# Optimization experiments

Hardware: AMD Instinct MI355X
Metric: run time of the kernel (lower is better)

## Reference

```python
import jax, jax.numpy as jnp
import numpy as np

B, S, D, H, F = 2, 2048, 768, 12, 3072
DH = D // H  # head dim = 64


def setup_inputs() -> dict:
    key = jax.random.key(0)
    ks = jax.random.split(key, 16)
    sc = 0.02
    p = {
        "src": jax.random.normal(ks[0], (B, S, D), jnp.float32),
        # attention projections (torch Linear layout: [out, in], bias=True in xformers MultiHeadDispatch)
        "wq": jax.random.normal(ks[1], (D, D), jnp.float32) * sc,
        "bq": jnp.zeros((D,), jnp.float32),
        "wk": jax.random.normal(ks[2], (D, D), jnp.float32) * sc,
        "bk": jnp.zeros((D,), jnp.float32),
        "wv": jax.random.normal(ks[3], (D, D), jnp.float32) * sc,
        "bv": jnp.zeros((D,), jnp.float32),
        "wo": jax.random.normal(ks[4], (D, D), jnp.float32) * sc,
        "bo": jnp.zeros((D,), jnp.float32),
        # FFN: fc1 (bias) -> SwiGLU (two bias-free F->F projections) -> fc2 (bias)
        "w_fc1": jax.random.normal(ks[5], (F, D), jnp.float32) * sc,
        "b_fc1": jnp.zeros((F,), jnp.float32),
        "w_in": jax.random.normal(ks[6], (F, F), jnp.float32) * sc,
        "w_gate": jax.random.normal(ks[7], (F, F), jnp.float32) * sc,
        "w_fc2": jax.random.normal(ks[8], (D, F), jnp.float32) * sc,
        "b_fc2": jnp.zeros((D,), jnp.float32),
        # RMSNorm weights
        "g_attn": jnp.ones((D,), jnp.float32),
        "g_ffn": jnp.ones((D,), jnp.float32),
    }
    return p


def _rmsnorm(x, g):
    eps = jnp.asarray(jnp.finfo(x.dtype).eps, x.dtype)
    return x * jax.lax.rsqrt(jnp.mean(x * x, axis=-1, keepdims=True) + eps) * g


def _rope_cos_sin(seq_len, dim, dtype):
    # xformers RotaryEmbedding: inv_freq over even indices, emb = cat(freqs, freqs)
    inv_freq = 1.0 / (10000.0 ** (jnp.arange(0, dim, 2, dtype=jnp.float32) / dim))
    freqs = jnp.arange(seq_len, dtype=jnp.float32)[:, None] * inv_freq[None, :]  # [S, dim/2]
    emb = jnp.concatenate([freqs, freqs], axis=-1)  # [S, dim]
    return jnp.cos(emb).astype(dtype), jnp.sin(emb).astype(dtype)


def _rotate_half(x):
    x1, x2 = jnp.split(x, 2, axis=-1)
    return jnp.concatenate([-x2, x1], axis=-1)


def _apply_rope(x, cos, sin):
    # x: [B, H, S, DH]; cos/sin: [S, DH]
    return x * cos[None, None] + _rotate_half(x) * sin[None, None]


def _block(src, wq, bq, wk, bk, wv, bv, wo, bo,
           w_fc1, b_fc1, w_in, w_gate, w_fc2, b_fc2, g_attn, g_ffn):
    b, s, d = src.shape
    x = _rmsnorm(src, g_attn)
    q = (x @ wq.T + bq).reshape(b, s, H, DH).transpose(0, 2, 1, 3)
    k = (x @ wk.T + bk).reshape(b, s, H, DH).transpose(0, 2, 1, 3)
    v = (x @ wv.T + bv).reshape(b, s, H, DH).transpose(0, 2, 1, 3)
    cos, sin = _rope_cos_sin(s, DH, x.dtype)
    q = _apply_rope(q, cos, sin)
    k = _apply_rope(k, cos, sin)
    scale = 1.0 / np.sqrt(DH)
    scores = jnp.einsum("bhsd,bhtd->bhst", q * scale, k)  # non-causal, no mask
    attn = jax.nn.softmax(scores, axis=-1)
    ctx = jnp.einsum("bhst,bhtd->bhsd", attn, v)
    ctx = ctx.transpose(0, 2, 1, 3).reshape(b, s, d)
    attn_out = ctx @ wo.T + bo

    y = _rmsnorm(src + attn_out, g_ffn)
    h = y @ w_fc1.T + b_fc1
    h = (h @ w_in.T) * jax.nn.silu(h @ w_gate.T)  # SwiGLU
    ffn_out = h @ w_fc2.T + b_fc2
    return y + ffn_out


def reference(src, wq, bq, wk, bk, wv, bv, wo, bo,
              w_fc1, b_fc1, w_in, w_gate, w_fc2, b_fc2, g_attn, g_ffn):
    return _block(src, wq, bq, wk, bk, wv, bv, wo, bo,
                  w_fc1, b_fc1, w_in, w_gate, w_fc2, b_fc2, g_attn, g_ffn)
```

## Files before the change

kernel.cpp:

```cpp
#include <hip/hip_runtime.h>

#define DEV static __device__ __forceinline__

typedef __attribute__((ext_vector_type(8))) short bf16x8;
typedef __attribute__((ext_vector_type(4))) short short4v;
typedef __attribute__((ext_vector_type(4))) float f32x4;

DEV f32x4 mfma16(bf16x8 a, bf16x8 b, f32x4 c){
  return __builtin_amdgcn_mfma_f32_16x16x32_bf16(a, b, c, 0, 0, 0);
}
DEV float bf2f(short s){ union{unsigned u; float f;} v; v.u=((unsigned)(unsigned short)s)<<16; return v.f; }
DEV short f2bf(float f){ union{float f; unsigned u;} v; v.f=f; unsigned r=v.u+0x7fffu+((v.u>>16)&1u); return (short)(r>>16); }
DEV void gload16(const void* g, void* l){
  __builtin_amdgcn_global_load_lds((const __attribute__((address_space(1))) void*)g,
                                   (__attribute__((address_space(3))) void*)l, 16, 0, 0);
}
DEV int cvtpk(float lo, float hi){
  int r; asm("v_cvt_pk_bf16_f32 %0, %1, %2" : "=v"(r) : "v"(lo), "v"(hi)); return r;
}

enum { EPI_QKV=4 };

__global__ void k_csmall(const float* __restrict__ p0, const float* __restrict__ p1,
                         const float* __restrict__ p2, const float* __restrict__ p3,
                         short* __restrict__ dst){
  int v = blockIdx.x * 256 + threadIdx.x;
  const float* src; int rel;
  if      (v < 147456){ src=p0; rel=v; }
  else if (v < 294912){ src=p1; rel=v-147456; }
  else if (v < 442368){ src=p2; rel=v-294912; }
  else                { src=p3; rel=v-442368; }
  float4 x = ((const float4*)src)[rel];
  short4v o; o.x=f2bf(x.x); o.y=f2bf(x.y); o.z=f2bf(x.z); o.w=f2bf(x.w);
  ((short4v*)dst)[v] = o;
}

__global__ void k_rmsnorm(const float* __restrict__ x, const float* __restrict__ g,
                          short* __restrict__ out){
  int row = blockIdx.x*4 + (threadIdx.x>>6);
  int lane = threadIdx.x & 63;
  const float* xr = x + (size_t)row*768;
  float4 v[3];
  float ss = 0.f;
  #pragma unroll
  for (int i=0;i<3;i++){
    v[i] = *(const float4*)(xr + i*256 + lane*4);
    ss += v[i].x*v[i].x + v[i].y*v[i].y + v[i].z*v[i].z + v[i].w*v[i].w;
  }
  #pragma unroll
  for (int d=32; d>0; d>>=1) ss += __shfl_xor(ss, d);
  float sc = rsqrtf(ss*(1.f/768.f) + 1.1920929e-7f);
  #pragma unroll
  for (int i=0;i<3;i++){
    int c0 = i*256 + lane*4;
    float4 gv = *(const float4*)(g + c0);
    short4v o;
    o.x = f2bf(v[i].x*sc*gv.x); o.y = f2bf(v[i].y*sc*gv.y);
    o.z = f2bf(v[i].z*sc*gv.z); o.w = f2bf(v[i].w*sc*gv.w);
    *(short4v*)(out + (size_t)row*768 + c0) = o;
  }
}

template<int EPI>
__launch_bounds__(256, 2)
__global__ void k_gemm(const short* __restrict__ Aptr, const short* __restrict__ Bptr,
                       void* __restrict__ Cout, const float* __restrict__ bias,
                       const void* __restrict__ aux, const float* __restrict__ bias2,
                       const float* __restrict__ bias3, const void* __restrict__ aux2,
                       int M, int N, int K){
  __shared__ short ldsA[128*32];
  __shared__ short ldsB[128*32];
  const int t = threadIdx.x;
  const int wave = t >> 6, lane = t & 63;
  const int l15 = lane & 15, l4 = lane >> 4;
  const int nwg = gridDim.x * gridDim.y;
  const int bid0 = blockIdx.y * gridDim.x + blockIdx.x;
  const int cpx = nwg >> 3;
  const int bid = (bid0 & 7) * cpx + (bid0 >> 3);
  const int bm = bid / gridDim.x, bn = bid % gridDim.x;
  const int wr = wave >> 1, wc = wave & 1;

  f32x4 acc[4][4] = {};

  const short* Ag = Aptr + (size_t)(bm*128 + wave*32 + (lane>>2))*K + (lane&3)*8;
  const short* Bg = Bptr + (size_t)(bn*128 + wave*32 + (lane>>2))*K + (lane&3)*8;
  short* lA = ldsA + wave*1024;
  short* lB = ldsB + wave*1024;

  for (int k0 = 0; k0 < K; k0 += 32){
    __syncthreads();
    gload16(Ag + k0,                lA);
    gload16(Ag + k0 + 16*(size_t)K, lA + 512);
    gload16(Bg + k0,                lB);
    gload16(Bg + k0 + 16*(size_t)K, lB + 512);
    __syncthreads();
    bf16x8 af[4], bfr[4];
    #pragma unroll
    for (int m=0;m<4;m++) af[m]  = *(const bf16x8*)(ldsA + (wr*64 + m*16 + l15)*32 + l4*8);
    #pragma unroll
    for (int n=0;n<4;n++) bfr[n] = *(const bf16x8*)(ldsB + (wc*64 + n*16 + l15)*32 + l4*8);
    #pragma unroll
    for (int m=0;m<4;m++)
      #pragma unroll
      for (int n=0;n<4;n++)
        acc[m][n] = mfma16(af[m], bfr[n], acc[m][n]);
  }

  const int row0 = bm*128 + wr*64;
  const int col0 = bn*128 + wc*64;

  if constexpr (EPI == EPI_QKV){
    const int proj = col0 / 768;
    const int c768 = col0 - proj*768;
    const int h = c768 >> 6;
    const float* bs = proj==0 ? bias : (proj==1 ? bias2 : bias3);
    float bvv[4];
    #pragma unroll
    for (int n=0;n<4;n++) bvv[n] = bs[c768 + n*16 + l15];
    if (proj == 2){
      short* Ov = (short*)const_cast<void*>(aux2);
      #pragma unroll
      for (int m=0;m<4;m++){
        #pragma unroll
        for (int j=0;j<4;j++){
          int row = row0 + m*16 + l4*4 + j;
          int b = row >> 11, s = row & 2047;
          size_t hb = (size_t)(b*12 + h)*64;
          #pragma unroll
          for (int n=0;n<4;n++)
            Ov[(hb + n*16 + l15)*2048 + s] = f2bf(acc[m][n][j] + bvv[n]);
        }
      }
    } else {
      short* O = proj==0 ? (short*)Cout : (short*)const_cast<void*>(aux);
      const float sc = proj==0 ? 0.18033688011112042f : 1.0f;
      const float RC = 0.41524101186092034f;
      float invf0 = exp2f(-(float)l15 * RC);
      float invf1 = exp2f(-(float)(16 + l15) * RC);
      #pragma unroll
      for (int m=0;m<4;m++){
        #pragma unroll
        for (int j=0;j<4;j++){
          int row = row0 + m*16 + l4*4 + j;
          int b = row >> 11, s = row & 2047;
          size_t obase = ((size_t)(b*12 + h)*2048 + (size_t)s)*64;
          float a0 = acc[m][0][j] + bvv[0];
          float a1 = acc[m][1][j] + bvv[1];
          float a2 = acc[m][2][j] + bvv[2];
          float a3 = acc[m][3][j] + bvv[3];
          float sn0, cs0, sn1, cs1;
          __sincosf((float)s * invf0, &sn0, &cs0);
          __sincosf((float)s * invf1, &sn1, &cs1);
          O[obase + l15]      = f2bf((a0*cs0 - a2*sn0)*sc);
          O[obase + 16 + l15] = f2bf((a1*cs1 - a3*sn1)*sc);
          O[obase + 32 + l15] = f2bf((a2*cs0 + a0*sn0)*sc);
          O[obase + 48 + l15] = f2bf((a3*cs1 + a1*sn1)*sc);
        }
      }
    }
  }
}

__launch_bounds__(256, 4)
__global__ void k_fatA(const short* __restrict__ Q, const short* __restrict__ Kb,
                       const short* __restrict__ Vb, short* __restrict__ ctx,
                       const float* __restrict__ winf, const float* __restrict__ wgf,
                       const float* __restrict__ wfc2f, short* __restrict__ dstbig,
                       const float* __restrict__ wfc1, short* __restrict__ wfc1T){
  __shared__ short shm[16384];
  const int id = blockIdx.x;
  const int tid = threadIdx.x;

  if (id < 768){
    const int wave = tid>>6, lane = tid&63;
    const int l15 = lane&15, l4 = lane>>4;
    const int qt = id & 31, bh = id >> 5;
    const short* Qh  = Q  + (size_t)bh*2048*64;
    const short* Kh  = Kb + (size_t)bh*2048*64;
    const short* Vth = Vb + (size_t)bh*64*2048;

    const int r7  = lane>>3;
    const int swz = ((lane&7) ^ r7) << 3;
    const int rr0 = wave*8 + r7, rr1 = 32 + wave*8 + r7;
    const size_t kOff0 = (size_t)rr0*64   + swz, kOff1 = (size_t)rr1*64   + swz;
    const size_t vOff0 = (size_t)rr0*2048 + swz, vOff1 = (size_t)rr1*2048 + swz;

    bf16x8 qf[2];
    #pragma unroll
    for (int kf=0;kf<2;kf++)
      qf[kf] = *(const bf16x8*)(Qh + (size_t)(qt*64 + wave*16 + l15)*64 + kf*32 + l4*8);

    f32x4 cacc[4] = {};
    f32x4 lacc = {};
    union { int w[4]; bf16x8 v; } onesf;
    onesf.w[0] = onesf.w[1] = onesf.w[2] = onesf.w[3] = 0x3F803F80;

    #define STAGE(sel, kv0) do { \
      const short* ksp = Kh + (size_t)(kv0)*64; \
      const short* vsp = Vth + (kv0); \
      short* kd = shm + (sel)*4096 + wave*512; \
      short* vd = shm + 8192 + (sel)*4096 + wave*512; \
      gload16(ksp + kOff0, kd); \
      gload16(ksp + kOff1, kd + 2048); \
      gload16(vsp + vOff0, vd); \
      gload16(vsp + vOff1, vd + 2048); \
    } while(0)

    STAGE(0, 0);

    for (int tt = 0; tt < 32; ++tt){
      const int cur = tt & 1;
      if (tt < 31){
        STAGE(cur^1, (tt+1)*64);
        asm volatile("s_waitcnt vmcnt(4)" ::: "memory");
      } else {
        asm volatile("s_waitcnt vmcnt(0)" ::: "memory");
      }
      __builtin_amdgcn_sched_barrier(0);
      __builtin_amdgcn_s_barrier();
      __builtin_amdgcn_sched_barrier(0);

      const short* KtC = shm + cur*4096;
      const short* VtC = shm + 8192 + cur*4096;

      f32x4 sacc[4] = {};
      __builtin_amdgcn_s_setprio(1);
      #pragma unroll
      for (int kf=0;kf<2;kf++){
        #pragma unroll
        for (int mk=0;mk<4;mk++){
          int r = mk*16 + l15;
          bf16x8 kfr = *(const bf16x8*)(KtC + r*64 + (((kf*4+l4) ^ (l15&7))<<3));
          sacc[mk] = mfma16(kfr, qf[kf], sacc[mk]);
        }
      }
      __builtin_amdgcn_s_setprio(0);

      int pk01[4], pk23[4];
      #pragma unroll
      for (int mk=0;mk<4;mk++){
        float p0 = exp2f(sacc[mk][0]);
        float p1 = exp2f(sacc[mk][1]);
        float p2 = exp2f(sacc[mk][2]);
        float p3 = exp2f(sacc[mk][3]);
        pk01[mk] = cvtpk(p0, p1);
        pk23[mk] = cvtpk(p2, p3);
      }

      #pragma unroll
      for (int ks=0;ks<2;ks++){
        int srcA = l15 + ((l4&1)<<5);
        int srcB = srcA + 16;
        int hi = l4>>1;
        int w0a = __shfl(pk01[2*ks], srcA), w0b = __shfl(pk01[2*ks+1], srcA);
        int w1a = __shfl(pk23[2*ks], srcA), w1b = __shfl(pk23[2*ks+1], srcA);
        int w2a = __shfl(pk01[2*ks], srcB), w2b = __shfl(pk01[2*ks+1], srcB);
        int w3a = __shfl(pk23[2*ks], srcB), w3b = __shfl(pk23[2*ks+1], srcB);
        union { int w[4]; bf16x8 v; } pa;
        pa.w[0] = hi ? w0b : w0a;
        pa.w[1] = hi ? w1b : w1a;
        pa.w[2] = hi ? w2b : w2a;
        pa.w[3] = hi ? w3b : w3a;
        __builtin_amdgcn_s_setprio(1);
        #pragma unroll
        for (int nf=0;nf<4;nf++){
          int dh = nf*16 + l15;
          bf16x8 vf = *(const bf16x8*)(VtC + dh*64 + (((ks*4+l4) ^ (dh&7))<<3));
          cacc[nf] = mfma16(pa.v, vf, cacc[nf]);
        }
        lacc = mfma16(pa.v, onesf.v, lacc);
        __builtin_amdgcn_s_setprio(0);
      }

      __builtin_amdgcn_sched_barrier(0);
      __builtin_amdgcn_s_barrier();
    }
    #undef STAGE

    const int b = bh/12, h = bh%12;
    #pragma unroll
    for (int j=0;j<4;j++){
      float inv = 1.f / lacc[j];
      int s = qt*64 + wave*16 + l4*4 + j;
      size_t base = ((size_t)b*2048 + s)*768 + h*64;
      #pragma unroll
      for (int nf=0;nf<4;nf++)
        ctx[base + nf*16 + l15] = f2bf(cacc[nf][j] * inv);
    }
  } else if (id < 21504){
    int v = (id - 768)*256 + tid;
    const float* src; int rel;
    if      (v < 2359296){ src=winf;  rel=v; }
    else if (v < 4718592){ src=wgf;   rel=v-2359296; }
    else                 { src=wfc2f; rel=v-4718592; }
    float4 x = ((const float4*)src)[rel];
    short4v o; o.x=f2bf(x.x); o.y=f2bf(x.y); o.z=f2bf(x.z); o.w=f2bf(x.w);
    ((short4v*)dstbig)[v] = o;
  } else {
    int idx = id - 21504;
    int f0 = (idx % 96)*32, d0 = (idx / 96)*32;
    float* lt = (float*)shm;
    int r = tid >> 3, c4 = tid & 7;
    float4 v = *(const float4*)(wfc1 + (size_t)(f0 + r)*768 + d0 + c4*4);
    lt[r*33 + c4*4+0] = v.x; lt[r*33 + c4*4+1] = v.y;
    lt[r*33 + c4*4+2] = v.z; lt[r*33 + c4*4+3] = v.w;
    __syncthreads();
    short4v o;
    o.x = f2bf(lt[(c4*4+0)*33 + r]);
    o.y = f2bf(lt[(c4*4+1)*33 + r]);
    o.z = f2bf(lt[(c4*4+2)*33 + r]);
    o.w = f2bf(lt[(c4*4+3)*33 + r]);
    *(short4v*)(wfc1T + (size_t)(d0 + r)*3072 + f0 + c4*4) = o;
  }
}

__launch_bounds__(256, 2)
__global__ void k_fatB(const short* __restrict__ ctxb, const short* __restrict__ wo_b,
                       float* __restrict__ resid, const float* __restrict__ bo,
                       const float* __restrict__ srcf,
                       const short* __restrict__ win_b, const short* __restrict__ wfc1T,
                       short* __restrict__ Pw,
                       const float* __restrict__ bfc1, float* __restrict__ bvg){
  __shared__ short shm[8192];
  const int id = blockIdx.x;
  const int t = threadIdx.x;
  const int wave = t >> 6, lane = t & 63;
  const int l15 = lane & 15, l4 = lane >> 4;
  const int wr = wave >> 1, wc = wave & 1;
  short* lA = shm + wave*1024;
  short* lB = shm + 4096 + wave*1024;

  if (id < 192){
    const int bid = (id & 7)*24 + (id >> 3);
    const int bm = bid / 6, bn = bid % 6;
    f32x4 acc[4][4] = {};
    const short* Ag = ctxb + (size_t)(bm*128 + wave*32 + (lane>>2))*768 + (lane&3)*8;
    const short* Bg = wo_b + (size_t)(bn*128 + wave*32 + (lane>>2))*768 + (lane&3)*8;
    for (int k0 = 0; k0 < 768; k0 += 32){
      __syncthreads();
      gload16(Ag + k0,          lA);
      gload16(Ag + k0 + 16*768, lA + 512);
      gload16(Bg + k0,          lB);
      gload16(Bg + k0 + 16*768, lB + 512);
      __syncthreads();
      bf16x8 af[4], bfr[4];
      #pragma unroll
      for (int m=0;m<4;m++) af[m]  = *(const bf16x8*)(shm + (wr*64 + m*16 + l15)*32 + l4*8);
      #pragma unroll
      for (int n=0;n<4;n++) bfr[n] = *(const bf16x8*)(shm + 4096 + (wc*64 + n*16 + l15)*32 + l4*8);
      #pragma unroll
      for (int m=0;m<4;m++)
        #pragma unroll
        for (int n=0;n<4;n++)
          acc[m][n] = mfma16(af[m], bfr[n], acc[m][n]);
    }
    const int row0 = bm*128 + wr*64;
    const int col0 = bn*128 + wc*64;
    float bvv[4];
    #pragma unroll
    for (int n=0;n<4;n++) bvv[n] = bo[col0 + n*16 + l15];
    #pragma unroll
    for (int m=0;m<4;m++)
      #pragma unroll
      for (int j=0;j<4;j++){
        size_t rb = (size_t)(row0 + m*16 + l4*4 + j)*768 + col0 + l15;
        #pragma unroll
        for (int n=0;n<4;n++) resid[rb + n*16] = acc[m][n][j] + bvv[n] + srcf[rb + n*16];
      }
  } else if (id < 768){
    const int id2 = id - 192;
    const int z = id2 / 288;
    const int rest = id2 - z*288;
    const int koff = z * 1536;
    const int bid = (rest & 7)*36 + (rest >> 3);
    const int bm = bid / 6, bn = bid % 6;
    f32x4 acc[4][4] = {};
    const short* Ag = win_b + (size_t)(bm*128 + wave*32 + (lane>>2))*3072 + (lane&3)*8 + koff;
    const short* Bg = wfc1T + (size_t)(bn*128 + wave*32 + (lane>>2))*3072 + (lane&3)*8 + koff;
    for (int k0 = 0; k0 < 1536; k0 += 32){
      __syncthreads();
      gload16(Ag + k0,           lA);
      gload16(Ag + k0 + 16*3072, lA + 512);
      gload16(Bg + k0,           lB);
      gload16(Bg + k0 + 16*3072, lB + 512);
      __syncthreads();
      bf16x8 af[4], bfr[4];
      #pragma unroll
      for (int m=0;m<4;m++) af[m]  = *(const bf16x8*)(shm + (wr*64 + m*16 + l15)*32 + l4*8);
      #pragma unroll
      for (int n=0;n<4;n++) bfr[n] = *(const bf16x8*)(shm + 4096 + (wc*64 + n*16 + l15)*32 + l4*8);
      #pragma unroll
      for (int m=0;m<4;m++)
        #pragma unroll
        for (int n=0;n<4;n++)
          acc[m][n] = mfma16(af[m], bfr[n], acc[m][n]);
    }
    short* Pz = Pw + (size_t)z * 4718592;
    const int row0 = bm*128 + wr*64;
    const int col0 = bn*128 + wc*64;
    #pragma unroll
    for (int m=0;m<4;m++)
      #pragma unroll
      for (int j=0;j<4;j++){
        size_t rb = (size_t)(row0 + m*16 + l4*4 + j)*768 + col0 + l15;
        #pragma unroll
        for (int n=0;n<4;n++) Pz[rb + n*16] = f2bf(acc[m][n][j]);
      }
  } else {
    int row = (id - 768)*4 + wave;
    const short* wrow = win_b + (size_t)row*3072 + lane*48;
    const float* bb = bfc1 + lane*48;
    float s = 0.f;
    #pragma unroll
    for (int i=0;i<6;i++){
      bf16x8 w = *(const bf16x8*)(wrow + i*8);
      float4 b0 = *(const float4*)(bb + i*8);
      float4 b1 = *(const float4*)(bb + i*8 + 4);
      s += bf2f(w[0])*b0.x + bf2f(w[1])*b0.y + bf2f(w[2])*b0.z + bf2f(w[3])*b0.w
         + bf2f(w[4])*b1.x + bf2f(w[5])*b1.y + bf2f(w[6])*b1.z + bf2f(w[7])*b1.w;
    }
    #pragma unroll
    for (int d=32; d>0; d>>=1) s += __shfl_xor(s, d);
    if (lane == 0) bvg[row] = s;
  }
}

__global__ void k_fatC(const float* __restrict__ resid, const float* __restrict__ gffn,
                       short* __restrict__ yb,
                       const short* __restrict__ Pw, short* __restrict__ comp){
  const int id = blockIdx.x;
  if (id < 1024){
    int row = id*4 + (threadIdx.x>>6);
    int lane = threadIdx.x & 63;
    const float* xr = resid + (size_t)row*768;
    float4 v[3];
    float ss = 0.f;
    #pragma unroll
    for (int i=0;i<3;i++){
      v[i] = *(const float4*)(xr + i*256 + lane*4);
      ss += v[i].x*v[i].x + v[i].y*v[i].y + v[i].z*v[i].z + v[i].w*v[i].w;
    }
    #pragma unroll
    for (int d=32; d>0; d>>=1) ss += __shfl_xor(ss, d);
    float sc = rsqrtf(ss*(1.f/768.f) + 1.1920929e-7f);
    #pragma unroll
    for (int i=0;i<3;i++){
      int c0 = i*256 + lane*4;
      float4 gv = *(const float4*)(gffn + c0);
      short4v o;
      o.x = f2bf(v[i].x*sc*gv.x); o.y = f2bf(v[i].y*sc*gv.y);
      o.z = f2bf(v[i].z*sc*gv.z); o.w = f2bf(v[i].w*sc*gv.w);
      *(short4v*)(yb + (size_t)row*768 + c0) = o;
    }
  } else {
    int i = (id - 1024)*256 + threadIdx.x;
    short4v a = ((const short4v*)Pw)[i];
    short4v b = ((const short4v*)(Pw + 4718592))[i];
    short4v o;
    o.x = f2bf(bf2f(a.x) + bf2f(b.x)); o.y = f2bf(bf2f(a.y) + bf2f(b.y));
    o.z = f2bf(bf2f(a.z) + bf2f(b.z)); o.w = f2bf(bf2f(a.w) + bf2f(b.w));
    ((short4v*)comp)[i] = o;
  }
}

__launch_bounds__(256, 2)
__global__ void k_part(const short* __restrict__ Aptr, const short* __restrict__ Bptr,
                       short* __restrict__ Pa, short* __restrict__ Pb){
  __shared__ short ldsA[128*32];
  __shared__ short ldsB[128*32];
  const int t = threadIdx.x;
  const int wave = t >> 6, lane = t & 63;
  const int l15 = lane & 15, l4 = lane >> 4;
  const int K = 3072;
  const int z = blockIdx.z;
  const int koff = z * 768;
  const int bid0 = blockIdx.y * 6 + blockIdx.x;
  const int bid = (bid0 & 7) * 24 + (bid0 >> 3);
  const int bm = bid / 6, bn = bid % 6;
  const int wr = wave >> 1, wc = wave & 1;

  f32x4 acc[4][4] = {};

  const short* Ag = Aptr + (size_t)(bm*128 + wave*32 + (lane>>2))*K + (lane&3)*8 + koff;
  const short* Bg = Bptr + (size_t)(bn*128 + wave*32 + (lane>>2))*K + (lane&3)*8 + koff;
  short* lA = ldsA + wave*1024;
  short* lB = ldsB + wave*1024;

  for (int k0 = 0; k0 < 768; k0 += 32){
    __syncthreads();
    gload16(Ag + k0,                lA);
    gload16(Ag + k0 + 16*(size_t)K, lA + 512);
    gload16(Bg + k0,                lB);
    gload16(Bg + k0 + 16*(size_t)K, lB + 512);
    __syncthreads();
    bf16x8 af[4], bfr[4];
    #pragma unroll
    for (int m=0;m<4;m++) af[m]  = *(const bf16x8*)(ldsA + (wr*64 + m*16 + l15)*32 + l4*8);
    #pragma unroll
    for (int n=0;n<4;n++) bfr[n] = *(const bf16x8*)(ldsB + (wc*64 + n*16 + l15)*32 + l4*8);
    #pragma unroll
    for (int m=0;m<4;m++)
      #pragma unroll
      for (int n=0;n<4;n++)
        acc[m][n] = mfma16(af[m], bfr[n], acc[m][n]);
  }

  short* P = (z < 2) ? (Pa + (size_t)z*3145728) : (Pb + (size_t)(z-2)*3145728);
  const int row0 = bm*128 + wr*64;
  const int col0 = bn*128 + wc*64;
  #pragma unroll
  for (int m=0;m<4;m++)
    #pragma unroll
    for (int j=0;j<4;j++){
      size_t rb = (size_t)(row0 + m*16 + l4*4 + j)*768 + col0 + l15;
      #pragma unroll
      for (int n=0;n<4;n++) P[rb + n*16] = f2bf(acc[m][n][j]);
    }
}

__global__ void k_fc2red(const short* __restrict__ Pa, const short* __restrict__ Pb,
                         const float* __restrict__ bias, const short* __restrict__ yv,
                         float* __restrict__ out){
  int i = blockIdx.x * 256 + threadIdx.x;
  short4v a = ((const short4v*)Pa)[i];
  short4v b = ((const short4v*)(Pa + 3145728))[i];
  short4v c = ((const short4v*)Pb)[i];
  short4v d = ((const short4v*)(Pb + 3145728))[i];
  float4 bv = *(const float4*)(bias + (i % 192)*4);
  short4v y = ((const short4v*)yv)[i];
  float4 o;
  o.x = bf2f(a.x) + bf2f(b.x) + bf2f(c.x) + bf2f(d.x) + bv.x + bf2f(y.x);
  o.y = bf2f(a.y) + bf2f(b.y) + bf2f(c.y) + bf2f(d.y) + bv.y + bf2f(y.y);
  o.z = bf2f(a.z) + bf2f(b.z) + bf2f(c.z) + bf2f(d.z) + bv.z + bf2f(y.z);
  o.w = bf2f(a.w) + bf2f(b.w) + bf2f(c.w) + bf2f(d.w) + bv.w + bf2f(y.w);
  ((float4*)out)[i] = o;
}

__launch_bounds__(256, 2)
__global__ void k_ffglu(const short* __restrict__ Aptr, const short* __restrict__ Wcomp,
                        const float* __restrict__ bvg, short* __restrict__ Cout){
  __shared__ short lds[3*12288];
  const int tid = threadIdx.x;
  const int wave = tid >> 6, lane = tid & 63;
  const int l15 = lane & 15, l4 = lane >> 4;
  const int wm = wave >> 1, wn = wave & 1;
  const int K = 768, N = 3072;
  const int nt = 24;

  const int lin = blockIdx.y * 48 + blockIdx.x;
  const int xcd = lin & 7, idx = lin >> 3;
  const int bm = ((xcd & 1) << 3) + idx / 12;
  const int bn = (xcd >> 1) * 12 + idx % 12;

  const int srcC = ((lane & 3) ^ ((lane >> 3) & 3)) * 8;

  const short* aSrc[4];
  int aDst[4];
  #pragma unroll
  for (int i=0;i<4;i++){
    int s = i*4 + wave;
    int row = s*16 + (lane>>2);
    aSrc[i] = Aptr + (size_t)(bm*256 + row)*K + srcC;
    aDst[i] = s*512;
  }
  const short* bSrc[2];
  int bDst[2];
  #pragma unroll
  for (int i=0;i<2;i++){
    int j = i*4 + wave;
    int pidx = (j>>1)*16 + (lane>>2);
    int grow = (j & 1) ? 3072 : 0;
    bSrc[i] = Wcomp + (size_t)(grow + bn*64 + pidx)*K + srcC;
    bDst[i] = 8192 + j*512;
  }

  int offA[8], offB[4];
  #pragma unroll
  for (int m=0;m<8;m++){
    int r = wm*128 + m*16 + l15;
    offA[m] = r*32 + ((l4 ^ ((l15>>1)&3))<<3);
  }
  #pragma unroll
  for (int nf=0;nf<4;nf++){
    int r = wn*64 + nf*16 + l15;
    offB[nf] = 8192 + r*32 + ((l4 ^ ((l15>>1)&3))<<3);
  }

  f32x4 accv[8][2] = {};
  f32x4 accg[8][2] = {};

  short *b0 = lds, *b1 = lds + 12288, *b2 = lds + 24576;

  #define GSTAGE_ALL(buf, t) do{ \
    gload16(aSrc[0] + (size_t)(t)*32, (buf) + aDst[0]); \
    gload16(aSrc[1] + (size_t)(t)*32, (buf) + aDst[1]); \
    gload16(aSrc[2] + (size_t)(t)*32, (buf) + aDst[2]); \
    gload16(aSrc[3] + (size_t)(t)*32, (buf) + aDst[3]); \
    gload16(bSrc[0] + (size_t)(t)*32, (buf) + bDst[0]); \
    gload16(bSrc[1] + (size_t)(t)*32, (buf) + bDst[1]); \
  }while(0)

  GSTAGE_ALL(b0, 0);
  GSTAGE_ALL(b1, 1);

  for (int t = 0; t < nt; ++t){
    if (t < nt-1){
      asm volatile("s_waitcnt vmcnt(6)" ::: "memory");
    } else {
      asm volatile("s_waitcnt vmcnt(0)" ::: "memory");
    }
    __builtin_amdgcn_sched_barrier(0);
    __builtin_amdgcn_s_barrier();
    __builtin_amdgcn_sched_barrier(0);

    if (t + 2 < nt) GSTAGE_ALL(b2, t+2);

    bf16x8 a0 = *(const bf16x8*)(b0 + offA[0]);
    bf16x8 a1 = *(const bf16x8*)(b0 + offA[1]);
    bf16x8 a2 = *(const bf16x8*)(b0 + offA[2]);
    bf16x8 a3 = *(const bf16x8*)(b0 + offA[3]);
    bf16x8 a4 = *(const bf16x8*)(b0 + offA[4]);
    bf16x8 a5 = *(const bf16x8*)(b0 + offA[5]);
    bf16x8 a6 = *(const bf16x8*)(b0 + offA[6]);
    bf16x8 a7 = *(const bf16x8*)(b0 + offA[7]);
    bf16x8 v0 = *(const bf16x8*)(b0 + offB[0]);
    bf16x8 g0 = *(const bf16x8*)(b0 + offB[1]);
    bf16x8 v1 = *(const bf16x8*)(b0 + offB[2]);
    bf16x8 g1 = *(const bf16x8*)(b0 + offB[3]);

    __builtin_amdgcn_s_setprio(1);
    accv[0][0] = mfma16(a0, v0, accv[0][0]);  accg[0][0] = mfma16(a0, g0, accg[0][0]);
    accv[1][0] = mfma16(a1, v0, accv[1][0]);  accg[1][0] = mfma16(a1, g0, accg[1][0]);
    accv[2][0] = mfma16(a2, v0, accv[2][0]);  accg[2][0] = mfma16(a2, g0, accg[2][0]);
    accv[3][0] = mfma16(a3, v0, accv[3][0]);  accg[3][0] = mfma16(a3, g0, accg[3][0]);
    accv[0][1] = mfma16(a0, v1, accv[0][1]);  accg[0][1] = mfma16(a0, g1, accg[0][1]);
    accv[1][1] = mfma16(a1, v1, accv[1][1]);  accg[1][1] = mfma16(a1, g1, accg[1][1]);
    accv[2][1] = mfma16(a2, v1, accv[2][1]);  accg[2][1] = mfma16(a2, g1, accg[2][1]);
    accv[3][1] = mfma16(a3, v1, accv[3][1]);  accg[3][1] = mfma16(a3, g1, accg[3][1]);
    accv[4][0] = mfma16(a4, v0, accv[4][0]);  accg[4][0] = mfma16(a4, g0, accg[4][0]);
    accv[5][0] = mfma16(a5, v0, accv[5][0]);  accg[5][0] = mfma16(a5, g0, accg[5][0]);
    accv[6][0] = mfma16(a6, v0, accv[6][0]);  accg[6][0] = mfma16(a6, g0, accg[6][0]);
    accv[7][0] = mfma16(a7, v0, accv[7][0]);  accg[7][0] = mfma16(a7, g0, accg[7][0]);
    accv[4][1] = mfma16(a4, v1, accv[4][1]);  accg[4][1] = mfma16(a4, g1, accg[4][1]);
    accv[5][1] = mfma16(a5, v1, accv[5][1]);  accg[5][1] = mfma16(a5, g1, accg[5][1]);
    accv[6][1] = mfma16(a6, v1, accv[6][1]);  accg[6][1] = mfma16(a6, g1, accg[6][1]);
    accv[7][1] = mfma16(a7, v1, accv[7][1]);  accg[7][1] = mfma16(a7, g1, accg[7][1]);
    __builtin_amdgcn_s_setprio(0);

    short* tmp = b0; b0 = b1; b1 = b2; b2 = tmp;
  }
  #undef GSTAGE_ALL

  const int row0 = bm*256 + wm*128;
  #pragma unroll
  for (int m=0;m<8;m++){
    #pragma unroll
    for (int j=0;j<4;j++){
      size_t rb = (size_t)(row0 + m*16 + l4*4 + j)*N + bn*64 + wn*32 + l15;
      #pragma unroll
      for (int p=0;p<2;p++){
        int c = bn*64 + wn*32 + p*16 + l15;
        float g = accg[m][p][j] + bvg[3072 + c];
        float v = accv[m][p][j] + bvg[c];
        Cout[rb + p*16] = f2bf(v * g / (1.f + __expf(-g)));
      }
    }
  }
}

extern "C" void kernel_launch(void* const* d_in, const int* in_sizes, int n_in,
                              void* d_out, int out_size, void* d_ws, size_t ws_size,
                              hipStream_t stream){
  (void)in_sizes; (void)n_in; (void)out_size;
  const float* src   = (const float*)d_in[0];
  const float* wq    = (const float*)d_in[1];
  const float* bq    = (const float*)d_in[2];
  const float* wk    = (const float*)d_in[3];
  const float* bk    = (const float*)d_in[4];
  const float* wv    = (const float*)d_in[5];
  const float* bv    = (const float*)d_in[6];
  const float* wo    = (const float*)d_in[7];
  const float* bo    = (const float*)d_in[8];
  const float* wfc1  = (const float*)d_in[9];
  const float* bfc1  = (const float*)d_in[10];
  const float* win   = (const float*)d_in[11];
  const float* wgate = (const float*)d_in[12];
  const float* wfc2  = (const float*)d_in[13];
  const float* bfc2  = (const float*)d_in[14];
  const float* gattn = (const float*)d_in[15];
  const float* gffn  = (const float*)d_in[16];

  char* ws = (char*)d_ws;
  constexpr size_t SZ_W768  = 768ull*768*2;
  constexpr size_t SZ_WFC   = 3072ull*768*2;
  constexpr size_t SZ_WFF   = 3072ull*3072*2;
  constexpr size_t SZ_ACT   = 4096ull*768*2;
  constexpr size_t SZ_ACTF  = 4096ull*768*4;
  constexpr size_t SZ_H     = 4096ull*3072*2;
  constexpr size_t OFF_WQ    = 0;
  constexpr size_t OFF_WK    = OFF_WQ + SZ_W768;
  constexpr size_t OFF_WV    = OFF_WK + SZ_W768;
  constexpr size_t OFF_WO    = OFF_WV + SZ_W768;
  constexpr size_t OFF_WFC1  = OFF_WO + SZ_W768;
  constexpr size_t OFF_WIN   = OFF_WFC1 + SZ_WFC;
  constexpr size_t OFF_WGATE = OFF_WIN + SZ_WFF;
  constexpr size_t OFF_WFC2  = OFF_WGATE + SZ_WFF;
  constexpr size_t OFF_XN    = OFF_WFC2 + SZ_WFC;
  constexpr size_t OFF_Q     = OFF_XN + SZ_ACT;
  constexpr size_t OFF_K     = OFF_Q + SZ_ACT;
  constexpr size_t OFF_V     = OFF_K + SZ_ACT;
  constexpr size_t OFF_RES   = OFF_V + SZ_ACT;
  constexpr size_t OFF_HIN   = OFF_RES + SZ_ACTF;
  constexpr size_t OFF_H2    = OFF_HIN + SZ_H;
  constexpr size_t WS_NEED   = OFF_H2 + SZ_H;
  if (ws_size < WS_NEED) return;

  constexpr size_t OFF_COMP  = OFF_HIN;
  constexpr size_t OFF_T     = OFF_HIN + 6144ull*768*2;
  constexpr size_t OFF_BVG   = OFF_T + 768ull*3072*2;

  short* wq_b    = (short*)(ws+OFF_WQ);
  short* win_b   = (short*)(ws+OFF_WIN);
  short* wfc2_b  = (short*)(ws+OFF_WFC2);
  short* wo_b    = (short*)(ws+OFF_WO);
  short* xn      = (short*)(ws+OFF_XN);
  short* ctxb    = (short*)(ws+OFF_XN);
  short* qb      = (short*)(ws+OFF_Q);
  short* yb      = (short*)(ws+OFF_Q);
  short* kb2     = (short*)(ws+OFF_K);
  short* vb2     = (short*)(ws+OFF_V);
  float* resid   = (float*)(ws+OFF_RES);
  short* comp    = (short*)(ws+OFF_COMP);
  short* wfc1T   = (short*)(ws+OFF_T);
  float* bvg     = (float*)(ws+OFF_BVG);
  short* h2      = (short*)(ws+OFF_H2);
  short* Pw      = (short*)(ws+OFF_H2);
  short* partA   = (short*)(ws+OFF_HIN);
  short* partB   = (short*)(ws+OFF_K);

  k_csmall<<<2304, 256, 0, stream>>>(wq, wk, wv, wo, wq_b);
  k_rmsnorm<<<1024, 256, 0, stream>>>(src, gattn, xn);

  k_gemm<EPI_QKV><<<dim3(18,32), 256, 0, stream>>>(xn, wq_b, qb, bq, kb2, bk, bv, vb2, 4096, 2304, 768);

  k_fatA<<<23808, 256, 0, stream>>>(qb, kb2, vb2, ctxb, win, wgate, wfc2, win_b, wfc1, wfc1T);

  k_fatB<<<2304, 256, 0, stream>>>(ctxb, wo_b, resid, bo, src, win_b, wfc1T, Pw, bfc1, bvg);

  k_fatC<<<5632, 256, 0, stream>>>(resid, gffn, yb, Pw, comp);

  k_ffglu<<<dim3(48,16), 256, 0, stream>>>(yb, comp, bvg, h2);

  k_part<<<dim3(6,32,4), 256, 0, stream>>>(h2, wfc2_b, partA, partB);
  k_fc2red<<<3072, 256, 0, stream>>>(partA, partB, bfc2, yb, (float*)d_out);
}
```

Baseline: 235.0 us.

## Merge weight cast and RMSNorm launches, vectorize V stores, raise fatA occupancy

Folds the weight-to-bf16 conversion kernel and the attention RMSNorm kernel into one launch whose blocks branch on block index, removing one kernel launch and its tail. In the QKV epilogue, the V-transposed output now writes four consecutive sequence positions as one 8-byte store instead of four scalar 2-byte stores. The fused attention/prep kernel's launch bound is raised from 4 to 5 blocks per CU, which caps register usage and may cause spills.

```diff
diff --git a/kernel.cpp b/kernel.cpp
--- a/kernel.cpp
+++ b/kernel.cpp
@@ -21,43 +21,46 @@
 
 enum { EPI_QKV=4 };
 
-__global__ void k_csmall(const float* __restrict__ p0, const float* __restrict__ p1,
-                         const float* __restrict__ p2, const float* __restrict__ p3,
-                         short* __restrict__ dst){
-  int v = blockIdx.x * 256 + threadIdx.x;
-  const float* src; int rel;
-  if      (v < 147456){ src=p0; rel=v; }
-  else if (v < 294912){ src=p1; rel=v-147456; }
-  else if (v < 442368){ src=p2; rel=v-294912; }
-  else                { src=p3; rel=v-442368; }
-  float4 x = ((const float4*)src)[rel];
-  short4v o; o.x=f2bf(x.x); o.y=f2bf(x.y); o.z=f2bf(x.z); o.w=f2bf(x.w);
-  ((short4v*)dst)[v] = o;
-}
-
-__global__ void k_rmsnorm(const float* __restrict__ x, const float* __restrict__ g,
-                          short* __restrict__ out){
-  int row = blockIdx.x*4 + (threadIdx.x>>6);
-  int lane = threadIdx.x & 63;
-  const float* xr = x + (size_t)row*768;
-  float4 v[3];
-  float ss = 0.f;
-  #pragma unroll
-  for (int i=0;i<3;i++){
-    v[i] = *(const float4*)(xr + i*256 + lane*4);
-    ss += v[i].x*v[i].x + v[i].y*v[i].y + v[i].z*v[i].z + v[i].w*v[i].w;
-  }
-  #pragma unroll
-  for (int d=32; d>0; d>>=1) ss += __shfl_xor(ss, d);
-  float sc = rsqrtf(ss*(1.f/768.f) + 1.1920929e-7f);
-  #pragma unroll
-  for (int i=0;i<3;i++){
-    int c0 = i*256 + lane*4;
-    float4 gv = *(const float4*)(g + c0);
-    short4v o;
-    o.x = f2bf(v[i].x*sc*gv.x); o.y = f2bf(v[i].y*sc*gv.y);
-    o.z = f2bf(v[i].z*sc*gv.z); o.w = f2bf(v[i].w*sc*gv.w);
-    *(short4v*)(out + (size_t)row*768 + c0) = o;
+__global__ void k_fatD(const float* __restrict__ p0, const float* __restrict__ p1,
+                       const float* __restrict__ p2, const float* __restrict__ p3,
+                       short* __restrict__ dst,
+                       const float* __restrict__ x, const float* __restrict__ g,
+                       short* __restrict__ out){
+  const int id = blockIdx.x;
+  const int tid = threadIdx.x;
+  if (id < 2304){
+    int v = id*256 + tid;
+    const float* src; int rel;
+    if      (v < 147456){ src=p0; rel=v; }
+    else if (v < 294912){ src=p1; rel=v-147456; }
+    else if (v < 442368){ src=p2; rel=v-294912; }
+    else                { src=p3; rel=v-442368; }
+    float4 xv = ((const float4*)src)[rel];
+    short4v o; o.x=f2bf(xv.x); o.y=f2bf(xv.y); o.z=f2bf(xv.z); o.w=f2bf(xv.w);
+    ((short4v*)dst)[v] = o;
+  } else {
+    int row = (id-2304)*4 + (tid>>6);
+    int lane = tid & 63;
+    const float* xr = x + (size_t)row*768;
+    float4 v[3];
+    float ss = 0.f;
+    #pragma unroll
+    for (int i=0;i<3;i++){
+      v[i] = *(const float4*)(xr + i*256 + lane*4);
+      ss += v[i].x*v[i].x + v[i].y*v[i].y + v[i].z*v[i].z + v[i].w*v[i].w;
+    }
+    #pragma unroll
+    for (int d=32; d>0; d>>=1) ss += __shfl_xor(ss, d);
+    float sc = rsqrtf(ss*(1.f/768.f) + 1.1920929e-7f);
+    #pragma unroll
+    for (int i=0;i<3;i++){
+      int c0 = i*256 + lane*4;
+      float4 gv = *(const float4*)(g + c0);
+      short4v o;
+      o.x = f2bf(v[i].x*sc*gv.x); o.y = f2bf(v[i].y*sc*gv.y);
+      o.z = f2bf(v[i].z*sc*gv.z); o.w = f2bf(v[i].w*sc*gv.w);
+      *(short4v*)(out + (size_t)row*768 + c0) = o;
+    }
   }
 }
 
@@ -121,14 +124,17 @@
       short* Ov = (short*)const_cast<void*>(aux2);
       #pragma unroll
       for (int m=0;m<4;m++){
+        int s0 = row0 + m*16 + l4*4;
+        int b = s0 >> 11, s = s0 & 2047;
+        size_t hb = (size_t)(b*12 + h)*64;
         #pragma unroll
-        for (int j=0;j<4;j++){
-          int row = row0 + m*16 + l4*4 + j;
-          int b = row >> 11, s = row & 2047;
-          size_t hb = (size_t)(b*12 + h)*64;
-          #pragma unroll
-          for (int n=0;n<4;n++)
-            Ov[(hb + n*16 + l15)*2048 + s] = f2bf(acc[m][n][j] + bvv[n]);
+        for (int n=0;n<4;n++){
+          short4v pk;
+          pk.x = f2bf(acc[m][n][0] + bvv[n]);
+          pk.y = f2bf(acc[m][n][1] + bvv[n]);
+          pk.z = f2bf(acc[m][n][2] + bvv[n]);
+          pk.w = f2bf(acc[m][n][3] + bvv[n]);
+          *(short4v*)(Ov + (hb + n*16 + l15)*2048 + s) = pk;
         }
       }
     } else {
@@ -161,7 +167,7 @@
   }
 }
 
-__launch_bounds__(256, 4)
+__launch_bounds__(256, 5)
 __global__ void k_fatA(const short* __restrict__ Q, const short* __restrict__ Kb,
                        const short* __restrict__ Vb, short* __restrict__ ctx,
                        const float* __restrict__ winf, const float* __restrict__ wgf,
@@ -738,8 +744,7 @@
   short* partA   = (short*)(ws+OFF_HIN);
   short* partB   = (short*)(ws+OFF_K);
 
-  k_csmall<<<2304, 256, 0, stream>>>(wq, wk, wv, wo, wq_b);
-  k_rmsnorm<<<1024, 256, 0, stream>>>(src, gattn, xn);
+  k_fatD<<<3328, 256, 0, stream>>>(wq, wk, wv, wo, wq_b, src, gattn, xn);
 
   k_gemm<EPI_QKV><<<dim3(18,32), 256, 0, stream>>>(xn, wq_b, qb, bq, kb2, bk, bv, vb2, 4096, 2304, 768);
 
```

After: 233.2 us. No clear change (-0.8%).
